# Kernel optimization log

Measured on AMD Instinct MI355X. Metric: run time of the kernel, lower is better.

## Reference

```python
import jax, jax.numpy as jnp
import numpy as np

INPUT_DIM = 1024
HIDDEN_DIM = 1024
FORGET_BIAS = 0.0


def setup_inputs() -> dict:
    key = jax.random.key(0)
    ks = jax.random.split(key, 8)
    x = jax.random.normal(ks[0], (1024, 32, INPUT_DIM), dtype=jnp.float32)
    state = jnp.zeros((1, 32, HIDDEN_DIM), dtype=jnp.float32)
    std = 0.1
    wm_z = std * jax.random.normal(ks[1], (HIDDEN_DIM, INPUT_DIM), dtype=jnp.float32)
    wm_f = std * jax.random.normal(ks[2], (HIDDEN_DIM, INPUT_DIM), dtype=jnp.float32)
    wv_z = std * jax.random.normal(ks[3], (1, HIDDEN_DIM), dtype=jnp.float32)
    wv_f = std * jax.random.normal(ks[4], (1, HIDDEN_DIM), dtype=jnp.float32)
    bias_z = std * jax.random.normal(ks[5], (1, HIDDEN_DIM), dtype=jnp.float32)
    bias_f = std * jax.random.normal(ks[6], (1, HIDDEN_DIM), dtype=jnp.float32) + FORGET_BIAS
    return {"x": x, "state": state, "wm_z": wm_z, "wm_f": wm_f,
            "wv_z": wv_z, "wv_f": wv_f, "bias_z": bias_z, "bias_f": bias_f}


def reference(x, state, wm_z, wm_f, wv_z, wv_f, bias_z, bias_f):
    # x: [slen, bsz, in_dim]; state: [1, bsz, hidden]
    hidden_prev = state[0]  # [bsz, hidden]
    # Pre-activation input projections (batched GEMM over all timesteps).
    out_z = jnp.einsum('sbi,hi->sbh', x, wm_z)  # [slen, bsz, hidden]
    out_f = jnp.einsum('sbi,hi->sbh', x, wm_f)

    def step(cell, zf):
        z_, f_ = zf
        z_part = jnp.tanh(z_ + wv_z * cell + bias_z)
        f_part = jax.nn.sigmoid(f_ + wv_f * cell + bias_f)
        new_cell = cell * f_part + (1.0 - f_part) * z_part
        return new_cell, new_cell

    _, new_cells = jax.lax.scan(step, hidden_prev, (out_z, out_f))
    return new_cells  # [slen, bsz, hidden]
```

## Files before the change

kernel.cpp:

```cpp
#include <hip/hip_runtime.h>
#include <hip/hip_fp16.h>

#define S_LEN 1024
#define BSZ   32
#define IN_DIM 1024
#define HID   1024
#define MDIM  (S_LEN*BSZ)
#define NDIM  (2*HID)
#define KDIM  IN_DIM

typedef __attribute__((ext_vector_type(8))) _Float16 half8;
typedef __attribute__((ext_vector_type(2))) _Float16 half2v;
typedef __attribute__((ext_vector_type(4))) float    floatx4;

__global__ void cvt_x_kernel(const float* __restrict__ x, _Float16* __restrict__ xh) {
    int idx = blockIdx.x * blockDim.x + threadIdx.x;
    const float4* src = (const float4*)x + (size_t)idx * 2;
    float4 a = src[0], b = src[1];
    half8 h;
    h[0] = (_Float16)a.x; h[1] = (_Float16)a.y; h[2] = (_Float16)a.z; h[3] = (_Float16)a.w;
    h[4] = (_Float16)b.x; h[5] = (_Float16)b.y; h[6] = (_Float16)b.z; h[7] = (_Float16)b.w;
    *((half8*)xh + idx) = h;
}

__global__ void cvt_w_kernel(const float* __restrict__ wz, const float* __restrict__ wf,
                             _Float16* __restrict__ wh) {
    int idx = blockIdx.x * blockDim.x + threadIdx.x;
    int e0 = idx * 8;
    int r   = e0 >> 10;
    int col = e0 & 1023;
    int g = r >> 5, sub = r & 31;
    const float* src = (sub < 16)
        ? wz + ((size_t)(g * 16 + sub)      * KDIM + col)
        : wf + ((size_t)(g * 16 + sub - 16) * KDIM + col);
    const float4* s4 = (const float4*)src;
    float4 a = s4[0], b = s4[1];
    half8 h;
    h[0] = (_Float16)a.x; h[1] = (_Float16)a.y; h[2] = (_Float16)a.z; h[3] = (_Float16)a.w;
    h[4] = (_Float16)b.x; h[5] = (_Float16)b.y; h[6] = (_Float16)b.z; h[7] = (_Float16)b.w;
    *((half8*)wh + idx) = h;
}

#define BM 128
#define BN 128
#define BK 32

__global__ void gemm_f16_kernel(const _Float16* __restrict__ A, const _Float16* __restrict__ B,
                                uint* __restrict__ zf) {
    __shared__ _Float16 As[BM * BK];
    __shared__ _Float16 Bs[BN * BK];

    const int tid  = threadIdx.x;
    const int lane = tid & 63;
    const int wv   = tid >> 6;

    const int flat   = blockIdx.x;
    const int xcd    = flat & 7;
    const int local  = flat >> 3;
    const int tile_m = (local >> 4) * 8 + xcd;
    const int tile_n = local & 15;
    const int m0  = tile_m * BM;
    const int n0g = tile_n * BN;

    const int wm = (wv >> 1) * 64;
    const int wn = (wv & 1) * 64;

    floatx4 acc[4][4] = {};

    const int fr = lane & 15;
    const int fk = (lane >> 4) * 8;

    for (int k0 = 0; k0 < KDIM; k0 += BK) {
        #pragma unroll
        for (int i = 0; i < 2; ++i) {
            int cb  = i * 256 + wv * 64;
            int c   = cb + lane;
            int row = c >> 2;
            int kc  = (c & 3) * 8;
            const _Float16* gp = A + (size_t)(m0 + row) * KDIM + k0 + kc;
            __builtin_amdgcn_global_load_lds(
                (const __attribute__((address_space(1))) void*)gp,
                (__attribute__((address_space(3))) void*)(As + (size_t)cb * 8), 16, 0, 0);
            const _Float16* gq = B + (size_t)(n0g + row) * KDIM + k0 + kc;
            __builtin_amdgcn_global_load_lds(
                (const __attribute__((address_space(1))) void*)gq,
                (__attribute__((address_space(3))) void*)(Bs + (size_t)cb * 8), 16, 0, 0);
        }
        __syncthreads();

        half8 af[4], bf[4];
        #pragma unroll
        for (int i = 0; i < 4; ++i)
            af[i] = *(const half8*)(As + (wm + i * 16 + fr) * BK + fk);
        #pragma unroll
        for (int j = 0; j < 4; ++j)
            bf[j] = *(const half8*)(Bs + (wn + j * 16 + fr) * BK + fk);

        #pragma unroll
        for (int i = 0; i < 4; ++i)
            #pragma unroll
            for (int j = 0; j < 4; ++j)
                acc[i][j] = __builtin_amdgcn_mfma_f32_16x16x32_f16(af[i], bf[j], acc[i][j], 0, 0, 0);
        __syncthreads();
    }

    const int orow  = (lane >> 4) * 4;
    const int ocol  = lane & 15;
    const int gbase = (n0g + wn) >> 5;
    #pragma unroll
    for (int i = 0; i < 4; ++i)
        #pragma unroll
        for (int p = 0; p < 2; ++p) {
            int h = (gbase + p) * 16 + ocol;
            #pragma unroll
            for (int r = 0; r < 4; ++r) {
                int row = m0 + wm + i * 16 + orow + r;
                half2v v;
                v[0] = (_Float16)acc[i][2 * p][r];
                v[1] = (_Float16)acc[i][2 * p + 1][r];
                *(half2v*)(zf + (size_t)row * HID + h) = v;
            }
        }
}

#define UNR 32
__global__ __launch_bounds__(64) void scan_kernel(
    const uint* __restrict__ zf, float* __restrict__ out,
    const float* __restrict__ state,
    const float* __restrict__ wvz, const float* __restrict__ wvf,
    const float* __restrict__ bz, const float* __restrict__ bfv) {
    const int t = blockIdx.x * 64 + threadIdx.x;
    const int h = t & (HID - 1);
    const int stride = BSZ * HID;

    float cell = state[t];
    const float az = wvz[h], afc = wvf[h], cz = bz[h], cf = bfv[h];

    const uint* p = zf + t;
    float* po = out + t;

    uint buf[UNR];
    #pragma unroll
    for (int u = 0; u < UNR; ++u) buf[u] = p[(size_t)u * stride];

    for (int s0 = 0; s0 < S_LEN; s0 += UNR) {
        uint nb[UNR];
        if (s0 + UNR < S_LEN) {
            #pragma unroll
            for (int u = 0; u < UNR; ++u)
                nb[u] = p[(size_t)(s0 + UNR + u) * stride];
        }
        #pragma unroll
        for (int u = 0; u < UNR; ++u) {
            half2v h2 = __builtin_bit_cast(half2v, buf[u]);
            float zpre = (float)h2[0] + az * cell + cz;
            float fpre = (float)h2[1] + afc * cell + cf;
            float ez = __expf(2.0f * zpre);
            float zp = (ez - 1.0f) * __builtin_amdgcn_rcpf(ez + 1.0f);
            float fp = __builtin_amdgcn_rcpf(1.0f + __expf(-fpre));
            cell = fmaf(cell - zp, fp, zp);
            po[(size_t)(s0 + u) * stride] = cell;
        }
        #pragma unroll
        for (int u = 0; u < UNR; ++u) buf[u] = nb[u];
    }
}

extern "C" void kernel_launch(void* const* d_in, const int* in_sizes, int n_in,
                              void* d_out, int out_size, void* d_ws, size_t ws_size,
                              hipStream_t stream) {
    const float* x      = (const float*)d_in[0];
    const float* state  = (const float*)d_in[1];
    const float* wm_z   = (const float*)d_in[2];
    const float* wm_f   = (const float*)d_in[3];
    const float* wv_z   = (const float*)d_in[4];
    const float* wv_f   = (const float*)d_in[5];
    const float* bias_z = (const float*)d_in[6];
    const float* bias_f = (const float*)d_in[7];
    float* out = (float*)d_out;

    char* ws = (char*)d_ws;
    _Float16* xh = (_Float16*)ws;
    _Float16* wh = (_Float16*)(ws + (size_t)MDIM * KDIM * sizeof(_Float16));
    uint* zf     = (uint*)(ws + (size_t)MDIM * KDIM * sizeof(_Float16)
                              + (size_t)NDIM * KDIM * sizeof(_Float16));

    cvt_x_kernel<<<(MDIM * KDIM) / (256 * 8), 256, 0, stream>>>(x, xh);
    cvt_w_kernel<<<(NDIM * KDIM) / (256 * 8), 256, 0, stream>>>(wm_z, wm_f, wh);

    gemm_f16_kernel<<<(MDIM / BM) * (NDIM / BN), 256, 0, stream>>>(xh, wh, zf);

    scan_kernel<<<MDIM / 64, 64, 0, stream>>>(zf, out, state, wv_z, wv_f, bias_z, bias_f);
}
```

Baseline: 455.0 us.

## Transpose preactivation layout to time-contiguous and swizzle GEMM LDS tiles

```diff
diff --git a/kernel.cpp b/kernel.cpp
--- a/kernel.cpp
+++ b/kernel.cpp
@@ -15,12 +15,16 @@
 
 __global__ void cvt_x_kernel(const float* __restrict__ x, _Float16* __restrict__ xh) {
     int idx = blockIdx.x * blockDim.x + threadIdx.x;
-    const float4* src = (const float4*)x + (size_t)idx * 2;
-    float4 a = src[0], b = src[1];
+    int e0 = idx * 8;
+    int row = e0 >> 10;
+    int col = e0 & 1023;
+    int s = row >> 5, b = row & 31;
+    const float4* src = (const float4*)(x + e0);
+    float4 a = src[0], bb = src[1];
     half8 h;
-    h[0] = (_Float16)a.x; h[1] = (_Float16)a.y; h[2] = (_Float16)a.z; h[3] = (_Float16)a.w;
-    h[4] = (_Float16)b.x; h[5] = (_Float16)b.y; h[6] = (_Float16)b.z; h[7] = (_Float16)b.w;
-    *((half8*)xh + idx) = h;
+    h[0] = (_Float16)a.x;  h[1] = (_Float16)a.y;  h[2] = (_Float16)a.z;  h[3] = (_Float16)a.w;
+    h[4] = (_Float16)bb.x; h[5] = (_Float16)bb.y; h[6] = (_Float16)bb.z; h[7] = (_Float16)bb.w;
+    *(half8*)(xh + (((size_t)((b << 10) | s)) << 10) + col) = h;
 }
 
 __global__ void cvt_w_kernel(const float* __restrict__ wz, const float* __restrict__ wf,
@@ -46,7 +50,7 @@
 #define BK 32
 
 __global__ void gemm_f16_kernel(const _Float16* __restrict__ A, const _Float16* __restrict__ B,
-                                uint* __restrict__ zf) {
+                                uint* __restrict__ zfT) {
     __shared__ _Float16 As[BM * BK];
     __shared__ _Float16 Bs[BN * BK];
 
@@ -68,7 +72,7 @@
     floatx4 acc[4][4] = {};
 
     const int fr = lane & 15;
-    const int fk = (lane >> 4) * 8;
+    const int fc = lane >> 4;
 
     for (int k0 = 0; k0 < KDIM; k0 += BK) {
         #pragma unroll
@@ -76,7 +80,7 @@
             int cb  = i * 256 + wv * 64;
             int c   = cb + lane;
             int row = c >> 2;
-            int kc  = (c & 3) * 8;
+            int kc  = ((c & 3) ^ ((row >> 1) & 3)) * 8;
             const _Float16* gp = A + (size_t)(m0 + row) * KDIM + k0 + kc;
             __builtin_amdgcn_global_load_lds(
                 (const __attribute__((address_space(1))) void*)gp,
@@ -90,11 +94,15 @@
 
         half8 af[4], bf[4];
         #pragma unroll
-        for (int i = 0; i < 4; ++i)
-            af[i] = *(const half8*)(As + (wm + i * 16 + fr) * BK + fk);
-        #pragma unroll
-        for (int j = 0; j < 4; ++j)
-            bf[j] = *(const half8*)(Bs + (wn + j * 16 + fr) * BK + fk);
+        for (int i = 0; i < 4; ++i) {
+            int R = wm + i * 16 + fr;
+            af[i] = *(const half8*)(As + R * BK + (fc ^ ((R >> 1) & 3)) * 8);
+        }
+        #pragma unroll
+        for (int j = 0; j < 4; ++j) {
+            int R = wn + j * 16 + fr;
+            bf[j] = *(const half8*)(Bs + R * BK + (fc ^ ((R >> 1) & 3)) * 8);
+        }
 
         #pragma unroll
         for (int i = 0; i < 4; ++i)
@@ -107,62 +115,70 @@
     const int orow  = (lane >> 4) * 4;
     const int ocol  = lane & 15;
     const int gbase = (n0g + wn) >> 5;
+    const int b_blk = m0 >> 10;
+    const int sbase = (m0 & 1023) + wm;
     #pragma unroll
     for (int i = 0; i < 4; ++i)
         #pragma unroll
         for (int p = 0; p < 2; ++p) {
             int h = (gbase + p) * 16 + ocol;
-            #pragma unroll
-            for (int r = 0; r < 4; ++r) {
-                int row = m0 + wm + i * 16 + orow + r;
-                half2v v;
-                v[0] = (_Float16)acc[i][2 * p][r];
-                v[1] = (_Float16)acc[i][2 * p + 1][r];
-                *(half2v*)(zf + (size_t)row * HID + h) = v;
-            }
-        }
-}
-
-#define UNR 32
+            int s = sbase + i * 16 + orow;
+            uint4 v;
+            half2v e0; e0[0] = (_Float16)acc[i][2*p][0]; e0[1] = (_Float16)acc[i][2*p+1][0];
+            half2v e1; e1[0] = (_Float16)acc[i][2*p][1]; e1[1] = (_Float16)acc[i][2*p+1][1];
+            half2v e2; e2[0] = (_Float16)acc[i][2*p][2]; e2[1] = (_Float16)acc[i][2*p+1][2];
+            half2v e3; e3[0] = (_Float16)acc[i][2*p][3]; e3[1] = (_Float16)acc[i][2*p+1][3];
+            v.x = __builtin_bit_cast(uint, e0);
+            v.y = __builtin_bit_cast(uint, e1);
+            v.z = __builtin_bit_cast(uint, e2);
+            v.w = __builtin_bit_cast(uint, e3);
+            *(uint4*)(zfT + (((size_t)((b_blk << 10) + h)) << 10) + s) = v;
+        }
+}
+
+#define UNR 64
+#define NG  (UNR / 4)
 __global__ __launch_bounds__(64) void scan_kernel(
-    const uint* __restrict__ zf, float* __restrict__ out,
+    const uint* __restrict__ zfT, float* __restrict__ out,
     const float* __restrict__ state,
     const float* __restrict__ wvz, const float* __restrict__ wvf,
     const float* __restrict__ bz, const float* __restrict__ bfv) {
     const int t = blockIdx.x * 64 + threadIdx.x;
     const int h = t & (HID - 1);
-    const int stride = BSZ * HID;
 
     float cell = state[t];
     const float az = wvz[h], afc = wvf[h], cz = bz[h], cf = bfv[h];
 
-    const uint* p = zf + t;
+    const uint4* p4 = (const uint4*)zfT + (size_t)t * (S_LEN / 4);
     float* po = out + t;
 
-    uint buf[UNR];
+    uint4 buf[NG], nb[NG];
     #pragma unroll
-    for (int u = 0; u < UNR; ++u) buf[u] = p[(size_t)u * stride];
+    for (int g = 0; g < NG; ++g) buf[g] = p4[g];
 
     for (int s0 = 0; s0 < S_LEN; s0 += UNR) {
-        uint nb[UNR];
         if (s0 + UNR < S_LEN) {
+            const uint4* pn = p4 + (s0 + UNR) / 4;
             #pragma unroll
-            for (int u = 0; u < UNR; ++u)
-                nb[u] = p[(size_t)(s0 + UNR + u) * stride];
-        }
-        #pragma unroll
-        for (int u = 0; u < UNR; ++u) {
-            half2v h2 = __builtin_bit_cast(half2v, buf[u]);
-            float zpre = (float)h2[0] + az * cell + cz;
-            float fpre = (float)h2[1] + afc * cell + cf;
-            float ez = __expf(2.0f * zpre);
-            float zp = (ez - 1.0f) * __builtin_amdgcn_rcpf(ez + 1.0f);
-            float fp = __builtin_amdgcn_rcpf(1.0f + __expf(-fpre));
-            cell = fmaf(cell - zp, fp, zp);
-            po[(size_t)(s0 + u) * stride] = cell;
-        }
-        #pragma unroll
-        for (int u = 0; u < UNR; ++u) buf[u] = nb[u];
+            for (int g = 0; g < NG; ++g) nb[g] = pn[g];
+        }
+        #pragma unroll
+        for (int g = 0; g < NG; ++g) {
+            uint ww[4] = {buf[g].x, buf[g].y, buf[g].z, buf[g].w};
+            #pragma unroll
+            for (int e = 0; e < 4; ++e) {
+                half2v h2 = __builtin_bit_cast(half2v, ww[e]);
+                float zpre = (float)h2[0] + az * cell + cz;
+                float fpre = (float)h2[1] + afc * cell + cf;
+                float ez = __expf(2.0f * zpre);
+                float zp = (ez - 1.0f) * __builtin_amdgcn_rcpf(ez + 1.0f);
+                float fp = __builtin_amdgcn_rcpf(1.0f + __expf(-fpre));
+                cell = fmaf(cell - zp, fp, zp);
+                po[(size_t)(s0 + g * 4 + e) * (BSZ * HID)] = cell;
+            }
+        }
+        #pragma unroll
+        for (int g = 0; g < NG; ++g) buf[g] = nb[g];
     }
 }
 
@@ -182,13 +198,13 @@
     char* ws = (char*)d_ws;
     _Float16* xh = (_Float16*)ws;
     _Float16* wh = (_Float16*)(ws + (size_t)MDIM * KDIM * sizeof(_Float16));
-    uint* zf     = (uint*)(ws + (size_t)MDIM * KDIM * sizeof(_Float16)
+    uint* zfT    = (uint*)(ws + (size_t)MDIM * KDIM * sizeof(_Float16)
                               + (size_t)NDIM * KDIM * sizeof(_Float16));
 
     cvt_x_kernel<<<(MDIM * KDIM) / (256 * 8), 256, 0, stream>>>(x, xh);
     cvt_w_kernel<<<(NDIM * KDIM) / (256 * 8), 256, 0, stream>>>(wm_z, wm_f, wh);
 
-    gemm_f16_kernel<<<(MDIM / BM) * (NDIM / BN), 256, 0, stream>>>(xh, wh, zf);
-
-    scan_kernel<<<MDIM / 64, 64, 0, stream>>>(zf, out, state, wv_z, wv_f, bias_z, bias_f);
-}
+    gemm_f16_kernel<<<(MDIM / BM) * (NDIM / BN), 256, 0, stream>>>(xh, wh, zfT);
+
+    scan_kernel<<<MDIM / 64, 64, 0, stream>>>(zfT, out, state, wv_z, wv_f, bias_z, bias_f);
+}
```

Measured after the change: 462.7 us. Within noise of the previous version (+1.7%).
